# Kernel tuning notes

Hardware: AMD Instinct MI355X
Metric: run time of the kernel (lower is better)

The kernel has to match this reference:

```python
import jax, jax.numpy as jnp
import numpy as np

VOXEL = 0.4        # args['voxel_size'][0] -> discrete_ratio
DOWNSAMPLE = 4     # args['downsample_rate']


def _affine_warp(feats, theta, H, W):
    """torch F.affine_grid + F.grid_sample (bilinear, zeros padding, align_corners=False).
    feats: (N, C, H, W), theta: (N, 2, 3) -> (N, C, H, W)"""
    xs = (2.0 * jnp.arange(W, dtype=feats.dtype) + 1.0) / W - 1.0   # (W,)
    ys = (2.0 * jnp.arange(H, dtype=feats.dtype) + 1.0) / H - 1.0   # (H,)
    gx, gy = jnp.meshgrid(xs, ys)                                   # (H, W) each
    base = jnp.stack([gx, gy, jnp.ones_like(gx)], axis=-1)          # (H, W, 3)
    src = jnp.einsum('nij,hwj->nhwi', theta, base)                  # (N, H, W, 2) normalized coords
    px = (src[..., 0] + 1.0) * W / 2.0 - 0.5                        # pixel coords
    py = (src[..., 1] + 1.0) * H / 2.0 - 0.5

    def sample_one(im, x, y):  # im (C,H,W); x,y (H,W)
        x0 = jnp.floor(x)
        y0 = jnp.floor(y)
        wx = x - x0
        wy = y - y0
        out = jnp.zeros((im.shape[0],) + x.shape, im.dtype)
        for dy, wyy in ((0, 1.0 - wy), (1, wy)):
            for dx, wxx in ((0, 1.0 - wx), (1, wx)):
                xi = x0 + dx
                yi = y0 + dy
                valid = (xi >= 0) & (xi < W) & (yi >= 0) & (yi < H)
                xi_c = jnp.clip(xi, 0, W - 1).astype(jnp.int32)
                yi_c = jnp.clip(yi, 0, H - 1).astype(jnp.int32)
                v = im[:, yi_c, xi_c]  # (C, H, W) gather
                out = out + v * (wxx * wyy * valid)[None]
        return out

    return jax.vmap(sample_one)(feats, px, py)


def setup_inputs() -> dict:
    key = jax.random.key(0)
    k1, k2, k3, k4 = jax.random.split(key, 4)
    B, L, K = 2, 5, 5
    C, H, W = 64, 100, 252
    record_len = jnp.array([5, 3], dtype=jnp.int32)   # sum = 8 agents
    total = int(8 * K)                                 # 40 feature maps
    x = jax.random.normal(k1, (total, C, H, W), dtype=jnp.float32)
    rm = jax.random.normal(k2, (total, 2, H, W), dtype=jnp.float32)
    # near-identity 4x4 transforms so sampling stays mostly in-bounds
    eye = jnp.eye(4, dtype=jnp.float32)
    pairwise_t_matrix = eye + 0.1 * jax.random.normal(k3, (B, L, K, 4, 4), dtype=jnp.float32)
    time_diffs = jax.random.uniform(k4, (total,), dtype=jnp.float32)
    return {"x": x, "rm": rm, "pairwise_t_matrix": pairwise_t_matrix,
            "time_diffs": time_diffs, "record_len": record_len}


def reference(x, rm, pairwise_t_matrix, time_diffs, record_len):
    # rm / time_diffs unused in the non-communication MAX path (kept for fidelity)
    C, H, W = x.shape[1], x.shape[2], x.shape[3]
    B, L, K = pairwise_t_matrix.shape[:3]
    # slice 4x4 -> 2x3 affine: rows [0,1], cols [0,1,3]
    M = pairwise_t_matrix[:, :, :, 0:2, :][..., jnp.array([0, 1, 3])]  # (B,L,K,2,3)
    s = DOWNSAMPLE * VOXEL
    mult = jnp.array([[1.0, H / W, 2.0 / (s * W)],
                      [W / H, 1.0, 2.0 / (s * H)]], dtype=x.dtype)
    M = M * mult
    rl = np.asarray(record_len)               # static ragged agent counts
    starts = np.concatenate([[0], np.cumsum(rl)]) * K
    fused = []
    for b in range(B):                        # loop over small batch dim (ragged N)
        N = int(rl[b])
        theta = M[b, :N].reshape(-1, 2, 3)                    # (N*K, 2, 3)
        feats = x[int(starts[b]): int(starts[b]) + N * K]     # (N*K, C, H, W)
        warped = _affine_warp(feats, theta, H, W)             # (N*K, C, H, W)
        fused.append(jnp.max(warped, axis=0))                 # max over agents*frames
    return jnp.stack(fused)                   # (B, C, H, W)
```

## Files before the change

kernel.cpp:

```cpp
#include <hip/hip_runtime.h>


#define C_   64
#define H_   100
#define W_   252
#define L_   5
#define K_   5
#define CPT  4
#define SCALE 1.6f

__global__ __launch_bounds__(256)
void raindrop_fuse_kernel(const float* __restrict__ x,
                          const float* __restrict__ T,
                          const int*   __restrict__ record_len,
                          float* __restrict__ out)
{
    const int cg  = blockIdx.x;
    const int h   = blockIdx.y;
    const int b   = blockIdx.z;
    const int tid = threadIdx.x;

    __shared__ float th[L_ * K_][6];
    __shared__ int   s_start, s_NK;

    if (tid == 0) {
        int start = 0;
        for (int i = 0; i < b; ++i) start += record_len[i];
        s_start = start * K_;
        s_NK    = record_len[b] * K_;
    }
    if (tid < L_ * K_) {
        const int l = tid / K_, k = tid % K_;
        const float* t = T + (((size_t)(b * L_ + l) * K_ + k) << 4);
        th[tid][0] = t[0];
        th[tid][1] = t[1] * ((float)H_ / (float)W_);
        th[tid][2] = t[3] * (2.0f / (SCALE * (float)W_));
        th[tid][3] = t[4] * ((float)W_ / (float)H_);
        th[tid][4] = t[5];
        th[tid][5] = t[7] * (2.0f / (SCALE * (float)H_));
    }
    __syncthreads();

    const int w = tid;
    if (w >= W_) return;

    const float gx = (2.0f * (float)w + 1.0f) / (float)W_ - 1.0f;
    const float gy = (2.0f * (float)h + 1.0f) / (float)H_ - 1.0f;

    const int NK = s_NK;
    const int c0 = cg * CPT;
    const float* __restrict__ base =
        x + ((size_t)s_start * C_ + c0) * (size_t)(H_ * W_);

    float acc[CPT];
#pragma unroll
    for (int j = 0; j < CPT; ++j) acc[j] = -INFINITY;

    for (int n = 0; n < NK; ++n) {
        const float t00 = th[n][0], t01 = th[n][1], t02 = th[n][2];
        const float t10 = th[n][3], t11 = th[n][4], t12 = th[n][5];

        const float sx = t00 * gx + t01 * gy + t02;
        const float sy = t10 * gx + t11 * gy + t12;
        const float px = (sx + 1.0f) * (0.5f * (float)W_) - 0.5f;
        const float py = (sy + 1.0f) * (0.5f * (float)H_) - 0.5f;

        const float x0f = floorf(px), y0f = floorf(py);
        const float wx = px - x0f,   wy = py - y0f;
        const int x0 = (int)x0f, y0 = (int)y0f;
        const int x1 = x0 + 1,   y1 = y0 + 1;

        const bool vx0 = (x0 >= 0) & (x0 < W_);
        const bool vx1 = (x1 >= 0) & (x1 < W_);
        const bool vy0 = (y0 >= 0) & (y0 < H_);
        const bool vy1 = (y1 >= 0) & (y1 < H_);

        const float w00 = (1.0f - wx) * (1.0f - wy) * ((vx0 & vy0) ? 1.0f : 0.0f);
        const float w01 = wx          * (1.0f - wy) * ((vx1 & vy0) ? 1.0f : 0.0f);
        const float w10 = (1.0f - wx) * wy          * ((vx0 & vy1) ? 1.0f : 0.0f);
        const float w11 = wx          * wy          * ((vx1 & vy1) ? 1.0f : 0.0f);

        const int xc0 = min(max(x0, 0), W_ - 1);
        const int xc1 = min(max(x1, 0), W_ - 1);
        const int yc0 = min(max(y0, 0), H_ - 1);
        const int yc1 = min(max(y1, 0), H_ - 1);

        const int o00 = yc0 * W_ + xc0;
        const int o01 = yc0 * W_ + xc1;
        const int o10 = yc1 * W_ + xc0;
        const int o11 = yc1 * W_ + xc1;

        const float* __restrict__ p = base + (size_t)n * C_ * (size_t)(H_ * W_);
#pragma unroll
        for (int j = 0; j < CPT; ++j) {
            const float v = p[o00] * w00 + p[o01] * w01 +
                            p[o10] * w10 + p[o11] * w11;
            acc[j] = fmaxf(acc[j], v);
            p += H_ * W_;
        }
    }

    const size_t ob = ((size_t)(b * C_ + c0) * H_ + h) * (size_t)W_ + w;
#pragma unroll
    for (int j = 0; j < CPT; ++j)
        out[ob + (size_t)j * (H_ * W_)] = acc[j];
}

extern "C" void kernel_launch(void* const* d_in, const int* in_sizes, int n_in,
                              void* d_out, int out_size, void* d_ws, size_t ws_size,
                              hipStream_t stream) {
    const float* x          = (const float*)d_in[0];
    const float* T          = (const float*)d_in[2];
    const int*   record_len = (const int*)d_in[4];
    float*       out        = (float*)d_out;

    const int B = in_sizes[4];
    dim3 grid(C_ / CPT, H_, B);
    raindrop_fuse_kernel<<<grid, 256, 0, stream>>>(x, T, record_len, out);
}
```

Before: 437.6 us.

## Double-buffer bilinear sample loads and pair horizontal taps into 8-byte loads

```diff
diff --git a/kernel.cpp b/kernel.cpp
--- a/kernel.cpp
+++ b/kernel.cpp
@@ -8,6 +8,59 @@
 #define K_   5
 #define CPT  4
 #define SCALE 1.6f
+#define HW_  (H_ * W_)
+
+typedef struct __attribute__((aligned(4))) { float x, y; } f2u;
+
+__device__ __forceinline__ void stage_math(const float* __restrict__ thn,
+                                           float gx, float gy,
+                                           int& o0, int& o1,
+                                           float& wA0, float& wB0,
+                                           float& wA1, float& wB1)
+{
+    const float sx = thn[0] * gx + thn[1] * gy + thn[2];
+    const float sy = thn[3] * gx + thn[4] * gy + thn[5];
+    const float px = (sx + 1.0f) * (0.5f * (float)W_) - 0.5f;
+    const float py = (sy + 1.0f) * (0.5f * (float)H_) - 0.5f;
+
+    const float x0f = floorf(px), y0f = floorf(py);
+    const float wx = px - x0f,   wy = py - y0f;
+    const int x0 = (int)x0f, y0 = (int)y0f;
+    const int x1 = x0 + 1,   y1 = y0 + 1;
+
+    const bool vx0 = (x0 >= 0) & (x0 < W_);
+    const bool vx1 = (x1 >= 0) & (x1 < W_);
+    const bool vy0 = (y0 >= 0) & (y0 < H_);
+    const bool vy1 = (y1 >= 0) & (y1 < H_);
+
+    const float w00 = (1.0f - wx) * (1.0f - wy) * ((vx0 & vy0) ? 1.0f : 0.0f);
+    const float w01 = wx          * (1.0f - wy) * ((vx1 & vy0) ? 1.0f : 0.0f);
+    const float w10 = (1.0f - wx) * wy          * ((vx0 & vy1) ? 1.0f : 0.0f);
+    const float w11 = wx          * wy          * ((vx1 & vy1) ? 1.0f : 0.0f);
+
+    const int yc0 = min(max(y0, 0), H_ - 1);
+    const int yc1 = min(max(y1, 0), H_ - 1);
+    const int xp  = min(max(x0, 0), W_ - 2);
+
+    o0 = yc0 * W_ + xp;
+    o1 = yc1 * W_ + xp;
+
+    const bool sel = (x0 == xp);
+    wA0 = sel ? w00 : w01;  wB0 = sel ? w01 : w00;
+    wA1 = sel ? w10 : w11;  wB1 = sel ? w11 : w10;
+}
+
+__device__ __forceinline__ void issue_loads(const float* __restrict__ p,
+                                            int o0, int o1,
+                                            f2u* r0, f2u* r1)
+{
+#pragma unroll
+    for (int j = 0; j < CPT; ++j) {
+        r0[j] = *reinterpret_cast<const f2u*>(p + o0);
+        r1[j] = *reinterpret_cast<const f2u*>(p + o1);
+        p += HW_;
+    }
+}
 
 __global__ __launch_bounds__(256)
 void raindrop_fuse_kernel(const float* __restrict__ x,
@@ -50,60 +103,51 @@
     const int NK = s_NK;
     const int c0 = cg * CPT;
     const float* __restrict__ base =
-        x + ((size_t)s_start * C_ + c0) * (size_t)(H_ * W_);
+        x + ((size_t)s_start * C_ + c0) * (size_t)HW_;
 
     float acc[CPT];
 #pragma unroll
     for (int j = 0; j < CPT; ++j) acc[j] = -INFINITY;
 
-    for (int n = 0; n < NK; ++n) {
-        const float t00 = th[n][0], t01 = th[n][1], t02 = th[n][2];
-        const float t10 = th[n][3], t11 = th[n][4], t12 = th[n][5];
+    f2u  a0[CPT], a1[CPT], b0v[CPT], b1v[CPT];
+    float awA0, awB0, awA1, awB1;
+    float bwA0, bwB0, bwA1, bwB1;
+    int o0, o1;
 
-        const float sx = t00 * gx + t01 * gy + t02;
-        const float sy = t10 * gx + t11 * gy + t12;
-        const float px = (sx + 1.0f) * (0.5f * (float)W_) - 0.5f;
-        const float py = (sy + 1.0f) * (0.5f * (float)H_) - 0.5f;
+    stage_math(th[0], gx, gy, o0, o1, awA0, awB0, awA1, awB1);
+    issue_loads(base, o0, o1, a0, a1);
 
-        const float x0f = floorf(px), y0f = floorf(py);
-        const float wx = px - x0f,   wy = py - y0f;
-        const int x0 = (int)x0f, y0 = (int)y0f;
-        const int x1 = x0 + 1,   y1 = y0 + 1;
-
-        const bool vx0 = (x0 >= 0) & (x0 < W_);
-        const bool vx1 = (x1 >= 0) & (x1 < W_);
-        const bool vy0 = (y0 >= 0) & (y0 < H_);
-        const bool vy1 = (y1 >= 0) & (y1 < H_);
-
-        const float w00 = (1.0f - wx) * (1.0f - wy) * ((vx0 & vy0) ? 1.0f : 0.0f);
-        const float w01 = wx          * (1.0f - wy) * ((vx1 & vy0) ? 1.0f : 0.0f);
-        const float w10 = (1.0f - wx) * wy          * ((vx0 & vy1) ? 1.0f : 0.0f);
-        const float w11 = wx          * wy          * ((vx1 & vy1) ? 1.0f : 0.0f);
-
-        const int xc0 = min(max(x0, 0), W_ - 1);
-        const int xc1 = min(max(x1, 0), W_ - 1);
-        const int yc0 = min(max(y0, 0), H_ - 1);
-        const int yc1 = min(max(y1, 0), H_ - 1);
-
-        const int o00 = yc0 * W_ + xc0;
-        const int o01 = yc0 * W_ + xc1;
-        const int o10 = yc1 * W_ + xc0;
-        const int o11 = yc1 * W_ + xc1;
-
-        const float* __restrict__ p = base + (size_t)n * C_ * (size_t)(H_ * W_);
+    int n = 0;
+    while (true) {
+        if (n + 1 < NK) {
+            stage_math(th[n + 1], gx, gy, o0, o1, bwA0, bwB0, bwA1, bwB1);
+            issue_loads(base + (size_t)(n + 1) * C_ * HW_, o0, o1, b0v, b1v);
+        }
 #pragma unroll
         for (int j = 0; j < CPT; ++j) {
-            const float v = p[o00] * w00 + p[o01] * w01 +
-                            p[o10] * w10 + p[o11] * w11;
+            const float v = a0[j].x * awA0 + a0[j].y * awB0 +
+                            a1[j].x * awA1 + a1[j].y * awB1;
             acc[j] = fmaxf(acc[j], v);
-            p += H_ * W_;
         }
+        if (++n >= NK) break;
+
+        if (n + 1 < NK) {
+            stage_math(th[n + 1], gx, gy, o0, o1, awA0, awB0, awA1, awB1);
+            issue_loads(base + (size_t)(n + 1) * C_ * HW_, o0, o1, a0, a1);
+        }
+#pragma unroll
+        for (int j = 0; j < CPT; ++j) {
+            const float v = b0v[j].x * bwA0 + b0v[j].y * bwB0 +
+                            b1v[j].x * bwA1 + b1v[j].y * bwB1;
+            acc[j] = fmaxf(acc[j], v);
+        }
+        if (++n >= NK) break;
     }
 
     const size_t ob = ((size_t)(b * C_ + c0) * H_ + h) * (size_t)W_ + w;
 #pragma unroll
     for (int j = 0; j < CPT; ++j)
-        out[ob + (size_t)j * (H_ * W_)] = acc[j];
+        out[ob + (size_t)j * HW_] = acc[j];
 }
 
 extern "C" void kernel_launch(void* const* d_in, const int* in_sizes, int n_in,
```

Measured after the change: 398.1 us. 9.0% less time.
